# Kernel tuning notes

Measured on AMD Instinct MI355X. Metric: run time of the kernel, lower is better.

## Reference

```python
import jax, jax.numpy as jnp
import numpy as np

B, N, HN, HE, H = 8, 128, 256, 128, 8
DH = HN // H
P = N * (N - 1) // 2


def _ln(x, g, b, eps=1e-5):
    m = jnp.mean(x, axis=-1, keepdims=True)
    v = jnp.mean((x - m) ** 2, axis=-1, keepdims=True)
    return (x - m) * jax.lax.rsqrt(v + eps) * g + b


def setup_inputs() -> dict:
    key = jax.random.key(0)
    ks = jax.random.split(key, 16)
    i1, i2 = np.triu_indices(N, k=1)  # all unordered pairs, P = N(N-1)/2
    s = lambda fan: 1.0 / np.sqrt(fan)
    return {
        "node_feat": jax.random.normal(ks[0], (B, N, HN), jnp.float32),
        "edge_feat": jax.random.normal(ks[1], (B, P, HE), jnp.float32),
        "x_idx1": jnp.asarray(i1, jnp.int32),
        "x_idx2": jnp.asarray(i2, jnp.int32),
        "mask_valid": jax.random.bernoulli(ks[2], 0.9, (B, P)).astype(jnp.float32),
        "Wqkv": jax.random.normal(ks[3], (HN, 3 * HN), jnp.float32) * s(HN),
        "bqkv": jnp.zeros((3 * HN,), jnp.float32),
        "Wev": jax.random.normal(ks[4], (HE, HN), jnp.float32) * s(HE),
        "bev": jnp.zeros((HN,), jnp.float32),
        "Wea": jax.random.normal(ks[5], (HE, H), jnp.float32) * s(HE),
        "bea": jnp.zeros((H,), jnp.float32),
        "Wo": jax.random.normal(ks[6], (2 * HN, HN), jnp.float32) * s(2 * HN),
        "bo": jnp.zeros((HN,), jnp.float32),
        "Wsk": jax.random.normal(ks[7], (HN, 2 * HN), jnp.float32) * s(HN),
        "bsk": jnp.zeros((2 * HN,), jnp.float32),
        "gn": jnp.ones((HN,), jnp.float32),
        "bn": jnp.zeros((HN,), jnp.float32),
        "ge": jnp.ones((HE,), jnp.float32),
        "be": jnp.zeros((HE,), jnp.float32),
    }


def reference(node_feat, edge_feat, x_idx1, x_idx2, mask_valid,
              Wqkv, bqkv, Wev, bev, Wea, bea, Wo, bo, Wsk, bsk,
              gn, bn, ge, be):
    n_in = _ln(node_feat, gn, bn)                      # [B,N,HN]
    e_in = _ln(edge_feat, ge, be)                      # [B,P,HE]
    q, k, v = jnp.split(n_in @ Wqkv + bqkv, 3, axis=-1)
    to_h = lambda t: t.reshape(B, -1, H, DH).transpose(0, 2, 1, 3)
    q, k, v = to_h(q), to_h(k), to_h(v)                # [B,H,N,DH]
    e_val = to_h(e_in @ Wev + bev)                     # [B,H,P,DH]
    e_adj = (e_in @ Wea + bea).transpose(0, 2, 1)      # [B,H,P]

    scale = DH ** -0.5
    logits = jnp.einsum('bhqd,bhkd->bhqk', q, k) * scale  # [B,H,N,N]
    # per-pair logits; torch stacks [qk, edge_adj] then sums -> just add
    l_node1 = logits[:, :, x_idx1, x_idx2] + e_adj     # node i1 attends to i2
    l_node2 = logits[:, :, x_idx2, x_idx1] + e_adj     # node i2 attends to i1
    v_node1 = e_val + v[:, :, x_idx2]                  # value node i1 receives
    v_node2 = e_val + v[:, :, x_idx1]

    # group the 2P directed edges by destination node (= torch cat+sort+reshape)
    cat_idx = jnp.concatenate([x_idx1, x_idx2])        # [2P]
    order = jnp.argsort(cat_idx)                       # stable sort
    gl = jnp.concatenate([l_node1, l_node2], axis=2)[:, :, order].reshape(B, H, N, N - 1)
    gv = jnp.concatenate([v_node1, v_node2], axis=2)[:, :, order].reshape(B, H, N, N - 1, DH)
    gm = jnp.concatenate([mask_valid, mask_valid], axis=1)[:, order].reshape(B, N, N - 1)[:, None]  # [B,1,N,N-1]

    gl = jnp.where(gm == 0.0, -9e15, gl)
    probs = jax.nn.softmax(gl, axis=3)
    probs = probs * jnp.any(gm != 0.0, axis=3, keepdims=True).astype(probs.dtype)
    attn = jnp.einsum('bhnk,bhnkd->bhnd', probs, gv)   # [B,H,N,DH]
    attn = attn.transpose(0, 2, 1, 3).reshape(B, N, HN)

    comb = jax.nn.gelu(jnp.concatenate([n_in, attn], axis=-1) @ Wo + bo, approximate=False)
    val, gate = jnp.split(comb @ Wsk + bsk, 2, axis=-1)
    g = jax.nn.sigmoid(gate)
    return node_feat * (1.0 - g) + val * g
```

## Files before the change

### kernel.cpp

```cpp
#include <hip/hip_runtime.h>
#include <hip/hip_bf16.h>
#include <math.h>

#define BB 8
#define NN 128
#define HN 256
#define HE 128
#define NH 8
#define DH 32
#define PP 8128
#define BP (BB*PP)

typedef __hip_bfloat16 bf16;
typedef __hip_bfloat162 bf162;
typedef __attribute__((ext_vector_type(8))) short bf16x8;
typedef __attribute__((ext_vector_type(4))) float f32x4;

__device__ __forceinline__ float bf2f(bf16 x){ return __bfloat162float(x); }
__device__ __forceinline__ float bfraw2f(short u){
  return __uint_as_float(((unsigned)(unsigned short)u) << 16);
}

__device__ __forceinline__ float wave_sum(float v){
  #pragma unroll
  for (int off=32; off>=1; off>>=1) v += __shfl_xor(v, off, 64);
  return v;
}
__device__ __forceinline__ float g16_sum(float v){
  #pragma unroll
  for (int off=8; off>=1; off>>=1) v += __shfl_xor(v, off, 16);
  return v;
}

__device__ __forceinline__ int pair_idx(int a, int c){
  int i = a < c ? a : c;
  int j = a < c ? c : a;
  return ((i*(255 - i))>>1) + (j - i - 1);
}

#define C_NODE 0LL
#define C_MASK 262144LL
#define C_WQKV 327168LL
#define C_BQKV 523776LL
#define C_WEV  524544LL
#define C_BEV  557312LL
#define C_WEA  557568LL
#define C_BEA  558592LL
#define C_WO   558600LL
#define C_BO   689672LL
#define C_WSK  689928LL
#define C_BSK  821000LL
#define C_GN   821512LL
#define C_BN   821768LL
#define C_GE   822024LL
#define C_BE   822152LL
#define IOFF   822400LL
#define TOT8   102785
#define CONVBLKS 402
#define I_NIN  0LL
#define I_Q    262144LL
#define I_K    524288LL
#define I_V    786432LL
#define I_ATTN 1048576LL
#define I_COMB 1310720LL
#define I_EA2  1572864LL
#define I_XG   2093056LL
#define I_WT   14577664LL
#define I_WOB  14594048LL
#define I_WSKB 14659584LL
#define I_FLG  14725120LL

struct SrcPtrs { const void* p[16]; };

__global__ __launch_bounds__(256) void k_convert(SrcPtrs sp, float* __restrict__ dst,
                                                 int* __restrict__ flags,
                                                 const unsigned short* __restrict__ nodeRaw,
                                                 const void* __restrict__ rawWev,
                                                 bf16* __restrict__ Wt,
                                                 const void* __restrict__ rawWo,
                                                 const void* __restrict__ rawWsk,
                                                 bf16* __restrict__ WoB,
                                                 bf16* __restrict__ WskB)
{
  __shared__ int sbad;
  if (threadIdx.x == 0) sbad = 0;
  __syncthreads();
  {
    int bad = 0;
    for (int i = threadIdx.x; i < 1024; i += 256){
      unsigned e = (nodeRaw[i] >> 7) & 0xFFu;
      if (e >= 194u) bad = 1;
    }
    if (bad) sbad = 1;
  }
  __syncthreads();
  const int f32 = sbad;
  if (blockIdx.x == 0 && threadIdx.x == 0) flags[0] = f32;

  if (blockIdx.x >= CONVBLKS + 128){
    int o = (blockIdx.x - (CONVBLKS + 128))*256 + threadIdx.x;
    const void* src = (o < 16384) ? rawWo : rawWsk;
    bf16* dw = (o < 16384) ? WoB : WskB;
    int lo = (o < 16384) ? o : o - 16384;
    if (f32){
      const float4* s4 = (const float4*)src;
      float4 a0 = s4[2*lo], a1 = s4[2*lo+1];
      union { float4 f; bf16 h[8]; } cv;
      cv.h[0]=__float2bfloat16(a0.x); cv.h[1]=__float2bfloat16(a0.y);
      cv.h[2]=__float2bfloat16(a0.z); cv.h[3]=__float2bfloat16(a0.w);
      cv.h[4]=__float2bfloat16(a1.x); cv.h[5]=__float2bfloat16(a1.y);
      cv.h[6]=__float2bfloat16(a1.z); cv.h[7]=__float2bfloat16(a1.w);
      *reinterpret_cast<float4*>(dw + lo*8) = cv.f;
    } else {
      *reinterpret_cast<float4*>(dw + lo*8) = ((const float4*)src)[lo];
    }
    return;
  }

  if (blockIdx.x >= CONVBLKS){
    int idx = (blockIdx.x - CONVBLKS)*256 + threadIdx.x;
    float v = f32 ? ((const float*)rawWev)[idx]
                  : bfraw2f(((const short*)rawWev)[idx]);
    Wt[(idx & 255)*128 + (idx >> 8)] = __float2bfloat16(v);
    return;
  }

  int o = blockIdx.x*256 + threadIdx.x;
  if (o >= TOT8) return;
  const int cum[17] = {0,32768,40896,65472,65568,69664,69696,69824,69825,
                       86209,86241,102625,102689,102721,102753,102769,102785};
  int s = 0;
  #pragma unroll
  for (int i = 1; i <= 15; i++) if (o >= cum[i]) s = i;
  const int li = o - cum[s];
  float4 r0, r1;
  if (f32){
    const float4* src = (const float4*)sp.p[s];
    r0 = src[2*li]; r1 = src[2*li+1];
  } else {
    union { float4 f; unsigned short u[8]; } cv;
    cv.f = ((const float4*)sp.p[s])[li];
    r0.x = __uint_as_float((unsigned)cv.u[0] << 16);
    r0.y = __uint_as_float((unsigned)cv.u[1] << 16);
    r0.z = __uint_as_float((unsigned)cv.u[2] << 16);
    r0.w = __uint_as_float((unsigned)cv.u[3] << 16);
    r1.x = __uint_as_float((unsigned)cv.u[4] << 16);
    r1.y = __uint_as_float((unsigned)cv.u[5] << 16);
    r1.z = __uint_as_float((unsigned)cv.u[6] << 16);
    r1.w = __uint_as_float((unsigned)cv.u[7] << 16);
  }
  float4* d = (float4*)(dst + (long long)cum[s]*8);
  d[2*li]   = r0;
  d[2*li+1] = r1;
}

__global__ __launch_bounds__(256) void k1_node_ln_qkv(
    const float* __restrict__ cnode, const float* __restrict__ cWqkv,
    const float* __restrict__ cbqkv, const float* __restrict__ cgn, const float* __restrict__ cbn,
    float* __restrict__ nin_ws, float* __restrict__ q_ws, float* __restrict__ k_ws,
    float* __restrict__ v_ws)
{
  __shared__ float xln[4][HN];
  const int t = threadIdx.x, wv = t>>6, lane = t&63;
  const int cb = blockIdx.x % 3;
  const int g0 = (blockIdx.x / 3) * 4;
  {
    int g = g0 + wv;
    float x[4];
    #pragma unroll
    for (int i=0;i<4;i++) x[i] = cnode[g*HN + lane + 64*i];
    float s = x[0]+x[1]+x[2]+x[3];
    s = wave_sum(s);
    float m = s * (1.0f/HN);
    float q = 0.f;
    #pragma unroll
    for (int i=0;i<4;i++){ float d = x[i]-m; q += d*d; }
    q = wave_sum(q);
    float rstd = rsqrtf(fmaxf(q*(1.0f/HN), 0.f) + 1e-5f);
    #pragma unroll
    for (int i=0;i<4;i++){
      int c = lane + 64*i;
      float y = (x[i]-m)*rstd*cgn[c] + cbn[c];
      xln[wv][c] = y;
      if (cb == 0) nin_ws[g*HN + c] = y;
    }
  }
  __syncthreads();
  const int col = cb*256 + t;
  float acc[4];
  {
    float bb = cbqkv[col];
    #pragma unroll
    for (int r=0;r<4;r++) acc[r] = bb;
  }
  for (int k=0;k<HN;k+=4){
    float4 xv[4];
    #pragma unroll
    for (int r=0;r<4;r++) xv[r] = *reinterpret_cast<const float4*>(&xln[r][k]);
    #pragma unroll
    for (int kk=0;kk<4;kk++){
      float w = cWqkv[(k+kk)*768 + col];
      #pragma unroll
      for (int r=0;r<4;r++) acc[r] = fmaf((&xv[r].x)[kk], w, acc[r]);
    }
  }
  if (cb == 2){
    #pragma unroll
    for (int r=0;r<4;r++) v_ws[(long)(g0+r)*HN + t] = acc[r];
  } else {
    float* dstp = (cb == 0) ? q_ws : k_ws;
    const int h = t>>5, d = t&31;
    #pragma unroll
    for (int r=0;r<4;r++){
      int g = g0 + r;
      int b = g>>7, n = g&127;
      dstp[((b*NH + h)*NN + n)*DH + d] = acc[r];
    }
  }
}

__global__ __launch_bounds__(256) void k2a_edge_ln(
    const void* __restrict__ edge_raw, const float* __restrict__ cWea,
    const float* __restrict__ cbea, const float* __restrict__ cge,
    const float* __restrict__ cbe, const float* __restrict__ cmask,
    bf16* __restrict__ xg, float* __restrict__ ea2, const int* __restrict__ flags)
{
  __shared__ float xlnS[16][136];
  __shared__ float part[128];
  const int t = threadIdx.x;
  const int R0 = blockIdx.x*16;
  const int b = R0 / PP;
  const int p0 = R0 - b*PP;
  const int f32 = flags[0];
  {
    int r = t>>4, sub = t&15;
    long base = (long)(R0 + r)*HE + sub*8;
    float x[8];
    if (f32){
      const float* cef = (const float*)edge_raw + base;
      float4 a0 = *reinterpret_cast<const float4*>(cef);
      float4 a1 = *reinterpret_cast<const float4*>(cef + 4);
      x[0]=a0.x; x[1]=a0.y; x[2]=a0.z; x[3]=a0.w;
      x[4]=a1.x; x[5]=a1.y; x[6]=a1.z; x[7]=a1.w;
    } else {
      union { float4 f; short u[8]; } cv;
      cv.f = *reinterpret_cast<const float4*>((const bf16*)edge_raw + base);
      #pragma unroll
      for (int i=0;i<8;i++) x[i] = bfraw2f(cv.u[i]);
    }
    float s = 0.f;
    #pragma unroll
    for (int i=0;i<8;i++) s += x[i];
    s = g16_sum(s);
    float m = s*(1.0f/HE);
    float q = 0.f;
    #pragma unroll
    for (int i=0;i<8;i++){ float dd = x[i]-m; q += dd*dd; }
    q = g16_sum(q);
    float rstd = rsqrtf(fmaxf(q*(1.0f/HE), 0.f) + 1e-5f);
    #pragma unroll
    for (int i=0;i<8;i++){
      int c = sub*8 + i;
      xlnS[r][c] = (x[i]-m)*rstd*cge[c] + cbe[c];
    }
  }
  __syncthreads();
  {
    int r = t>>4, c0 = (t&15)*8;
    union { float4 f; bf16 h[8]; } o;
    #pragma unroll
    for (int i=0;i<8;i++) o.h[i] = __float2bfloat16(xlnS[r][c0+i]);
    *reinterpret_cast<float4*>(xg + (long)(R0 + r)*HE + c0) = o.f;
  }
  {
    const int c = t & 7, r = (t>>3) & 15, half = t>>7;
    const int pid = r*8 + c;
    float s = half ? 0.0f : cbea[c];
    const int k0 = half*64;
    #pragma unroll 8
    for (int k=k0; k<k0+64; k++) s = fmaf(xlnS[r][k], cWea[k*NH + c], s);
    if (half){ part[pid] = s; }
    __syncthreads();
    if (!half){
      s += part[pid];
      int p = p0 + r;
      float mk = cmask[b*PP + p];
      ea2[((long)b*PP + p)*8 + c] = (mk != 0.0f) ? s : -9e15f;
    }
  }
}

__global__ __launch_bounds__(256, 4) void k3_attn(
    const float* __restrict__ q_ws,
    const float* __restrict__ k_ws,
    const float* __restrict__ v_ws,
    const bf16* __restrict__ xg,
    const float* __restrict__ ea2,
    const bf16* __restrict__ Wt,
    const float* __restrict__ cbev,
    float* __restrict__ attn)
{
  __shared__ __align__(16) bf16  xgS[128][128];
  __shared__ __align__(16) float sS[8][128];
  const int t = threadIdx.x;
  const int bid = blockIdx.x;
  const int swz = (bid & 7)*128 + (bid >> 3);
  const int n = swz & 127, b = swz >> 7;
  const int h = t >> 5, ln = t & 31;

  float4 qv[8];
  const float* qb = q_ws + (((long)b*NH + h)*NN + n)*DH;
  #pragma unroll
  for (int d4=0; d4<8; d4++) qv[d4] = *reinterpret_cast<const float4*>(qb + d4*4);
  float eav[4];
  const float* eab = ea2 + (long)b*PP*8;
  #pragma unroll
  for (int j=0;j<4;j++){
    int m = ln + 32*j;
    int ms = (m == n) ? (m ^ 1) : m;
    eav[j] = eab[(long)pair_idx(n, ms)*8 + h];
  }
  const bf16* xgb = xg + (long)b*PP*HE;
  const int rowb = t >> 4, seg = t & 15;
  float4 xr[8];
  #pragma unroll
  for (int it=0; it<8; ++it){
    int row = it*16 + rowb;
    int ms = (row == n) ? (row ^ 1) : row;
    int pr = pair_idx(n, ms);
    xr[it] = *reinterpret_cast<const float4*>(xgb + (long)pr*HE + seg*8);
  }

  const float scale = 0.17677669529663687f;
  const float* kb = k_ws + ((long)b*NH + h)*NN*DH;
  float l[4];
  float mx = -INFINITY;
  int valid = 0;
  #pragma unroll
  for (int j=0;j<4;j++){
    int m = ln + 32*j;
    const float* kr = kb + m*DH;
    float dot = 0.f;
    #pragma unroll
    for (int d4=0; d4<8; d4++){
      float4 kv = *reinterpret_cast<const float4*>(kr + d4*4);
      dot = fmaf(qv[d4].x, kv.x, dot);
      dot = fmaf(qv[d4].y, kv.y, dot);
      dot = fmaf(qv[d4].z, kv.z, dot);
      dot = fmaf(qv[d4].w, kv.w, dot);
    }
    bool self = (m == n);
    l[j] = self ? -INFINITY : fmaf(dot, scale, eav[j]);
    if (!self && eav[j] > -8.9e15f) valid = 1;
    mx = fmaxf(mx, l[j]);
  }
  #pragma unroll
  for (int off=16; off>=1; off>>=1) mx = fmaxf(mx, __shfl_xor(mx, off, 32));
  float e[4], s = 0.f;
  #pragma unroll
  for (int j=0;j<4;j++){ e[j] = __expf(l[j]-mx); s += e[j]; }
  float av = valid ? 1.f : 0.f;
  #pragma unroll
  for (int off=16; off>=1; off>>=1){
    s  += __shfl_xor(s,  off, 32);
    av += __shfl_xor(av, off, 32);
  }
  float inv = (av > 0.f) ? (1.0f/s) : 0.f;
  float pj0 = e[0]*inv, pj1 = e[1]*inv, pj2 = e[2]*inv, pj3 = e[3]*inv;

  #pragma unroll
  for (int it=0; it<8; ++it){
    int row = it*16 + rowb;
    *reinterpret_cast<float4*>(&xgS[row][seg*8]) = xr[it];
  }
  __syncthreads();

  const float* vb = v_ws + (long)b*NN*HN + h*DH + ln;
  float S0=0.f,S1=0.f,S2=0.f,S3=0.f,T=0.f;
  #pragma unroll
  for (int j=0;j<4;j++){
    float pcur = (j==0) ? pj0 : (j==1) ? pj1 : (j==2) ? pj2 : pj3;
    #pragma unroll 2
    for (int mm=0; mm<32; mm+=4){
      #pragma unroll
      for (int i=0;i<4;i++){
        int m = j*32 + mm + i;
        float pm = __shfl(pcur, mm + i, 32);
        short4 xv = *reinterpret_cast<const short4*>(&xgS[m][ln*4]);
        S0 = fmaf(pm, bfraw2f(xv.x), S0);
        S1 = fmaf(pm, bfraw2f(xv.y), S1);
        S2 = fmaf(pm, bfraw2f(xv.z), S2);
        S3 = fmaf(pm, bfraw2f(xv.w), S3);
        T  = fmaf(pm, vb[m*HN], T);
      }
    }
  }
  {
    float4 sv; sv.x=S0; sv.y=S1; sv.z=S2; sv.w=S3;
    *reinterpret_cast<float4*>(&sS[h][ln*4]) = sv;
  }
  __syncthreads();

  float acc = T + ((av > 0.f) ? cbev[h*DH + ln] : 0.f);
  const bf16* wr = Wt + (h*DH + ln)*HE;
  #pragma unroll 4
  for (int k0=0;k0<128;k0+=8){
    float4 sa = *reinterpret_cast<const float4*>(&sS[h][k0]);
    float4 sb = *reinterpret_cast<const float4*>(&sS[h][k0+4]);
    bf16x8 wv = *reinterpret_cast<const bf16x8*>(wr + k0);
    acc = fmaf(sa.x, bfraw2f(wv[0]), acc);
    acc = fmaf(sa.y, bfraw2f(wv[1]), acc);
    acc = fmaf(sa.z, bfraw2f(wv[2]), acc);
    acc = fmaf(sa.w, bfraw2f(wv[3]), acc);
    acc = fmaf(sb.x, bfraw2f(wv[4]), acc);
    acc = fmaf(sb.y, bfraw2f(wv[5]), acc);
    acc = fmaf(sb.z, bfraw2f(wv[6]), acc);
    acc = fmaf(sb.w, bfraw2f(wv[7]), acc);
  }
  attn[((long)b*NN + n)*HN + h*DH + ln] = acc;
}

__global__ __launch_bounds__(256) void k4_wo_gelu(
    const float* __restrict__ nin_ws, const float* __restrict__ attn,
    const bf16* __restrict__ WoB, const float* __restrict__ cbo,
    float* __restrict__ comb)
{
  __shared__ float xc[4][512];
  __shared__ float ps[3][4][64];
  const int t = threadIdx.x;
  const int g0 = (blockIdx.x >> 2) * 4;
  const int cq = blockIdx.x & 3;
  {
    int r = t>>6, c0 = (t&63)*8;
    const float* src = (c0 < 256) ? (nin_ws + (long)(g0+r)*HN + c0)
                                  : (attn + (long)(g0+r)*HN + (c0-256));
    float4 a0 = *reinterpret_cast<const float4*>(src);
    float4 a1 = *reinterpret_cast<const float4*>(src+4);
    *reinterpret_cast<float4*>(&xc[r][c0]) = a0;
    *reinterpret_cast<float4*>(&xc[r][c0+4]) = a1;
  }
  __syncthreads();
  const int cidx = t & 63, ks = t >> 6;
  const int col = cq*64 + cidx;
  float acc[4] = {0.f,0.f,0.f,0.f};
  const int k0 = ks*128;
  #pragma unroll 4
  for (int k=k0; k<k0+128; k++){
    float w = bf2f(WoB[k*HN + col]);
    #pragma unroll
    for (int r=0;r<4;r++) acc[r] = fmaf(xc[r][k], w, acc[r]);
  }
  if (ks){
    #pragma unroll
    for (int r=0;r<4;r++) ps[ks-1][r][cidx] = acc[r];
  }
  __syncthreads();
  if (!ks){
    float bb = cbo[col];
    #pragma unroll
    for (int r=0;r<4;r++){
      float x = acc[r] + bb + ps[0][r][cidx] + ps[1][r][cidx] + ps[2][r][cidx];
      comb[(long)(g0+r)*HN + col] = 0.5f*x*(1.0f + erff(x*0.7071067811865475f));
    }
  }
}

__global__ __launch_bounds__(256) void k5_sk_gate(
    const float* __restrict__ comb, const float* __restrict__ cnode,
    const bf16* __restrict__ WskB, const float* __restrict__ cbsk,
    void* __restrict__ out, const int* __restrict__ flags)
{
  __shared__ float xc[4][HN];
  __shared__ float psv[3][4][64];
  __shared__ float psg[3][4][64];
  const int t = threadIdx.x;
  const int g0 = (blockIdx.x >> 2) * 4;
  const int cq = blockIdx.x & 3;
  {
    int r = t>>6, c0 = (t&63)*4;
    *reinterpret_cast<float4*>(&xc[r][c0]) =
        *reinterpret_cast<const float4*>(comb + (long)(g0+r)*HN + c0);
  }
  __syncthreads();
  const int cidx = t & 63, ks = t >> 6;
  const int col = cq*64 + cidx;
  float av[4] = {0.f,0.f,0.f,0.f}, ag[4] = {0.f,0.f,0.f,0.f};
  const int k0 = ks*64;
  #pragma unroll 4
  for (int k=k0; k<k0+64; k++){
    float wv = bf2f(WskB[k*512 + col]);
    float wg = bf2f(WskB[k*512 + col + 256]);
    #pragma unroll
    for (int r=0;r<4;r++){
      float xr = xc[r][k];
      av[r] = fmaf(xr, wv, av[r]);
      ag[r] = fmaf(xr, wg, ag[r]);
    }
  }
  if (ks){
    #pragma unroll
    for (int r=0;r<4;r++){ psv[ks-1][r][cidx] = av[r]; psg[ks-1][r][cidx] = ag[r]; }
  }
  __syncthreads();
  if (!ks){
    const int f32 = flags[0];
    float bv = cbsk[col], bg = cbsk[col+256];
    #pragma unroll
    for (int r=0;r<4;r++){
      float v = av[r] + bv + psv[0][r][cidx] + psv[1][r][cidx] + psv[2][r][cidx];
      float g = ag[r] + bg + psg[0][r][cidx] + psg[1][r][cidx] + psg[2][r][cidx];
      float gg = 1.0f/(1.0f + __expf(-g));
      float nf = cnode[(long)(g0+r)*HN + col];
      float res = nf*(1.0f - gg) + v*gg;
      if (f32) ((float*)out)[(long)(g0+r)*HN + col] = res;
      else ((bf16*)out)[(long)(g0+r)*HN + col] = __float2bfloat16(res);
    }
  }
}

extern "C" void kernel_launch(void* const* d_in, const int* in_sizes, int n_inputs,
                              void* d_out, int out_size, void* d_ws, size_t ws_size,
                              hipStream_t stream)
{
  float* ws = (float*)d_ws;
  float* c_node = ws + C_NODE;
  float* c_mask = ws + C_MASK;
  float* c_Wqkv = ws + C_WQKV;
  float* c_bqkv = ws + C_BQKV;
  float* c_bev  = ws + C_BEV;
  float* c_Wea  = ws + C_WEA;
  float* c_bea  = ws + C_BEA;
  float* c_bo   = ws + C_BO;
  float* c_bsk  = ws + C_BSK;
  float* c_gn   = ws + C_GN;
  float* c_bn   = ws + C_BN;
  float* c_ge   = ws + C_GE;
  float* c_be   = ws + C_BE;
  float* base   = ws + IOFF;
  float* nin_ws  = base + I_NIN;
  float* q_ws    = base + I_Q;
  float* k_ws    = base + I_K;
  float* v_ws    = base + I_V;
  float* attn_ws = base + I_ATTN;
  float* comb_ws = base + I_COMB;
  float* ea2_ws  = base + I_EA2;
  bf16*  xg_ws   = (bf16*)(base + I_XG);
  bf16*  wt_ws   = (bf16*)(base + I_WT);
  bf16*  wob_ws  = (bf16*)(base + I_WOB);
  bf16*  wskb_ws = (bf16*)(base + I_WSKB);
  int*   flags   = (int*)(base + I_FLG);

  SrcPtrs sp;
  sp.p[0]  = d_in[0];
  sp.p[1]  = d_in[4];
  sp.p[2]  = d_in[5];
  sp.p[3]  = d_in[6];
  sp.p[4]  = d_in[7];
  sp.p[5]  = d_in[8];
  sp.p[6]  = d_in[9];
  sp.p[7]  = d_in[10];
  sp.p[8]  = d_in[11];
  sp.p[9]  = d_in[12];
  sp.p[10] = d_in[13];
  sp.p[11] = d_in[14];
  sp.p[12] = d_in[15];
  sp.p[13] = d_in[16];
  sp.p[14] = d_in[17];
  sp.p[15] = d_in[18];

  k_convert<<<CONVBLKS + 256, 256, 0, stream>>>(sp, ws, flags,
                                                (const unsigned short*)d_in[0],
                                                d_in[7], wt_ws,
                                                d_in[11], d_in[13],
                                                wob_ws, wskb_ws);
  k1_node_ln_qkv<<<768, 256, 0, stream>>>(c_node, c_Wqkv, c_bqkv, c_gn, c_bn,
                                          nin_ws, q_ws, k_ws, v_ws);
  k2a_edge_ln<<<BP/16, 256, 0, stream>>>(d_in[1], c_Wea, c_bea, c_ge, c_be, c_mask,
                                         xg_ws, ea2_ws, flags);
  k3_attn<<<BB*NN, 256, 0, stream>>>(q_ws, k_ws, v_ws, xg_ws, ea2_ws, wt_ws, c_bev,
                                     attn_ws);
  k4_wo_gelu<<<1024, 256, 0, stream>>>(nin_ws, attn_ws, wob_ws, c_bo, comb_ws);
  k5_sk_gate<<<1024, 256, 0, stream>>>(comb_ws, c_node, wskb_ws, c_bsk, d_out, flags);
}
```

Baseline: 198.0 us.

## Merge conversion, node LN/QKV and edge LN into one launch; fuse Wo and gate kernels

Removes the separate fp32 staging kernel: the node, edge and weight-prep stages now read raw inputs directly, with dtype conversion done inline, and run as block ranges of a single launch. Each block detects the input dtype itself. The Wo+GELU and skip/gate kernels are merged so the comb intermediate stays in shared memory. The cost is fewer blocks (256) with the full K loop per thread and no split-K in the merged kernel, which may reduce parallelism in that stage.

```diff
diff --git a/kernel.cpp b/kernel.cpp
--- a/kernel.cpp
+++ b/kernel.cpp
@@ -38,25 +38,10 @@
   return ((i*(255 - i))>>1) + (j - i - 1);
 }
 
-#define C_NODE 0LL
-#define C_MASK 262144LL
-#define C_WQKV 327168LL
-#define C_BQKV 523776LL
-#define C_WEV  524544LL
 #define C_BEV  557312LL
-#define C_WEA  557568LL
-#define C_BEA  558592LL
-#define C_WO   558600LL
 #define C_BO   689672LL
-#define C_WSK  689928LL
 #define C_BSK  821000LL
-#define C_GN   821512LL
-#define C_BN   821768LL
-#define C_GE   822024LL
-#define C_BE   822152LL
 #define IOFF   822400LL
-#define TOT8   102785
-#define CONVBLKS 402
 #define I_NIN  0LL
 #define I_Q    262144LL
 #define I_K    524288LL
@@ -70,36 +55,221 @@
 #define I_WSKB 14659584LL
 #define I_FLG  14725120LL
 
+#define EDGEBLKS 4064
+#define NODEBLKS 768
+#define PREPBLKS 257
+
 struct SrcPtrs { const void* p[16]; };
 
-__global__ __launch_bounds__(256) void k_convert(SrcPtrs sp, float* __restrict__ dst,
-                                                 int* __restrict__ flags,
-                                                 const unsigned short* __restrict__ nodeRaw,
-                                                 const void* __restrict__ rawWev,
-                                                 bf16* __restrict__ Wt,
-                                                 const void* __restrict__ rawWo,
-                                                 const void* __restrict__ rawWsk,
-                                                 bf16* __restrict__ WoB,
-                                                 bf16* __restrict__ WskB)
+__device__ __forceinline__ int detect_f32(const unsigned short* nodeRaw, int* sbad){
+  if (threadIdx.x == 0) *sbad = 0;
+  __syncthreads();
+  int bad = 0;
+  for (int i = threadIdx.x; i < 1024; i += 256){
+    unsigned e = (nodeRaw[i] >> 7) & 0xFFu;
+    if (e >= 194u) bad = 1;
+  }
+  if (bad) *sbad = 1;
+  __syncthreads();
+  return *sbad;
+}
+
+__device__ __forceinline__ float dualf(const void* p, long i, int f32){
+  return f32 ? ((const float*)p)[i] : bfraw2f(((const short*)p)[i]);
+}
+
+__global__ __launch_bounds__(256) void kA(
+    SrcPtrs sp, const void* __restrict__ edge_raw,
+    float* __restrict__ nin_ws, float* __restrict__ q_ws, float* __restrict__ k_ws,
+    float* __restrict__ v_ws, bf16* __restrict__ xg, float* __restrict__ ea2,
+    bf16* __restrict__ Wt, bf16* __restrict__ WoB, bf16* __restrict__ WskB,
+    float* __restrict__ ws, int* __restrict__ flags)
 {
-  __shared__ int sbad;
-  if (threadIdx.x == 0) sbad = 0;
-  __syncthreads();
-  {
-    int bad = 0;
-    for (int i = threadIdx.x; i < 1024; i += 256){
-      unsigned e = (nodeRaw[i] >> 7) & 0xFFu;
-      if (e >= 194u) bad = 1;
-    }
-    if (bad) sbad = 1;
-  }
-  __syncthreads();
-  const int f32 = sbad;
-  if (blockIdx.x == 0 && threadIdx.x == 0) flags[0] = f32;
-
-  if (blockIdx.x >= CONVBLKS + 128){
-    int o = (blockIdx.x - (CONVBLKS + 128))*256 + threadIdx.x;
-    const void* src = (o < 16384) ? rawWo : rawWsk;
+  __shared__ __align__(16) float smemF[3330];
+  int* sbad = (int*)&smemF[3328];
+  const int t = threadIdx.x;
+  int bb = blockIdx.x;
+
+  if (bb < EDGEBLKS){
+    const int f32 = detect_f32((const unsigned short*)sp.p[0], sbad);
+    float* xlnS = smemF;
+    float* part = smemF + 2176;
+    float* WeaS = smemF + 2304;
+    {
+      int i0 = t*4;
+      if (f32){
+        *reinterpret_cast<float4*>(&WeaS[i0]) =
+            *reinterpret_cast<const float4*>((const float*)sp.p[6] + i0);
+      } else {
+        union { float2 f; short u[4]; } cv;
+        cv.f = *reinterpret_cast<const float2*>((const short*)sp.p[6] + i0);
+        WeaS[i0]   = bfraw2f(cv.u[0]); WeaS[i0+1] = bfraw2f(cv.u[1]);
+        WeaS[i0+2] = bfraw2f(cv.u[2]); WeaS[i0+3] = bfraw2f(cv.u[3]);
+      }
+    }
+    const int R0 = bb*16;
+    const int b = R0 / PP;
+    const int p0 = R0 - b*PP;
+    {
+      int r = t>>4, sub = t&15;
+      long base = (long)(R0 + r)*HE + sub*8;
+      float x[8];
+      if (f32){
+        const float* cef = (const float*)edge_raw + base;
+        float4 a0 = *reinterpret_cast<const float4*>(cef);
+        float4 a1 = *reinterpret_cast<const float4*>(cef + 4);
+        x[0]=a0.x; x[1]=a0.y; x[2]=a0.z; x[3]=a0.w;
+        x[4]=a1.x; x[5]=a1.y; x[6]=a1.z; x[7]=a1.w;
+      } else {
+        union { float4 f; short u[8]; } cv;
+        cv.f = *reinterpret_cast<const float4*>((const bf16*)edge_raw + base);
+        #pragma unroll
+        for (int i=0;i<8;i++) x[i] = bfraw2f(cv.u[i]);
+      }
+      float s = 0.f;
+      #pragma unroll
+      for (int i=0;i<8;i++) s += x[i];
+      s = g16_sum(s);
+      float m = s*(1.0f/HE);
+      float q = 0.f;
+      #pragma unroll
+      for (int i=0;i<8;i++){ float dd = x[i]-m; q += dd*dd; }
+      q = g16_sum(q);
+      float rstd = rsqrtf(fmaxf(q*(1.0f/HE), 0.f) + 1e-5f);
+      #pragma unroll
+      for (int i=0;i<8;i++){
+        int c = sub*8 + i;
+        float gev = dualf(sp.p[14], c, f32);
+        float bev = dualf(sp.p[15], c, f32);
+        xlnS[r*136 + c] = (x[i]-m)*rstd*gev + bev;
+      }
+    }
+    __syncthreads();
+    {
+      int r = t>>4, c0 = (t&15)*8;
+      union { float4 f; bf16 h[8]; } o;
+      #pragma unroll
+      for (int i=0;i<8;i++) o.h[i] = __float2bfloat16(xlnS[r*136 + c0+i]);
+      *reinterpret_cast<float4*>(xg + (long)(R0 + r)*HE + c0) = o.f;
+    }
+    {
+      const int c = t & 7, r = (t>>3) & 15, half = t>>7;
+      const int pid = r*8 + c;
+      float s = half ? 0.0f : dualf(sp.p[7], c, f32);
+      const int k0 = half*64;
+      #pragma unroll 8
+      for (int k=k0; k<k0+64; k++) s = fmaf(xlnS[r*136 + k], WeaS[k*NH + c], s);
+      if (half){ part[pid] = s; }
+      __syncthreads();
+      if (!half){
+        s += part[pid];
+        int p = p0 + r;
+        float mk = dualf(sp.p[1], (long)b*PP + p, f32);
+        ea2[((long)b*PP + p)*8 + c] = (mk != 0.0f) ? s : -9e15f;
+      }
+    }
+    return;
+  }
+  bb -= EDGEBLKS;
+
+  if (bb < NODEBLKS){
+    const int f32 = detect_f32((const unsigned short*)sp.p[0], sbad);
+    float* xln = smemF;
+    const int wv = t>>6, lane = t&63;
+    const int cb = bb % 3;
+    const int g0 = (bb / 3) * 4;
+    {
+      int g = g0 + wv;
+      float x[4];
+      if (f32){
+        const float* cn = (const float*)sp.p[0];
+        #pragma unroll
+        for (int i=0;i<4;i++) x[i] = cn[(long)g*HN + lane + 64*i];
+      } else {
+        const short* cn = (const short*)sp.p[0];
+        #pragma unroll
+        for (int i=0;i<4;i++) x[i] = bfraw2f(cn[(long)g*HN + lane + 64*i]);
+      }
+      float s = x[0]+x[1]+x[2]+x[3];
+      s = wave_sum(s);
+      float m = s * (1.0f/HN);
+      float q = 0.f;
+      #pragma unroll
+      for (int i=0;i<4;i++){ float d = x[i]-m; q += d*d; }
+      q = wave_sum(q);
+      float rstd = rsqrtf(fmaxf(q*(1.0f/HN), 0.f) + 1e-5f);
+      #pragma unroll
+      for (int i=0;i<4;i++){
+        int c = lane + 64*i;
+        float gnv = dualf(sp.p[12], c, f32);
+        float bnv = dualf(sp.p[13], c, f32);
+        float y = (x[i]-m)*rstd*gnv + bnv;
+        xln[wv*HN + c] = y;
+        if (cb == 0) nin_ws[(long)g*HN + c] = y;
+      }
+    }
+    __syncthreads();
+    const int col = cb*256 + t;
+    float acc[4];
+    {
+      float bb0 = dualf(sp.p[3], col, f32);
+      #pragma unroll
+      for (int r=0;r<4;r++) acc[r] = bb0;
+    }
+    if (f32){
+      const float* W = (const float*)sp.p[2];
+      for (int k=0;k<HN;k+=4){
+        float4 xv[4];
+        #pragma unroll
+        for (int r=0;r<4;r++) xv[r] = *reinterpret_cast<const float4*>(&xln[r*HN + k]);
+        #pragma unroll
+        for (int kk=0;kk<4;kk++){
+          float w = W[(long)(k+kk)*768 + col];
+          #pragma unroll
+          for (int r=0;r<4;r++) acc[r] = fmaf((&xv[r].x)[kk], w, acc[r]);
+        }
+      }
+    } else {
+      const short* W = (const short*)sp.p[2];
+      for (int k=0;k<HN;k+=4){
+        float4 xv[4];
+        #pragma unroll
+        for (int r=0;r<4;r++) xv[r] = *reinterpret_cast<const float4*>(&xln[r*HN + k]);
+        #pragma unroll
+        for (int kk=0;kk<4;kk++){
+          float w = bfraw2f(W[(long)(k+kk)*768 + col]);
+          #pragma unroll
+          for (int r=0;r<4;r++) acc[r] = fmaf((&xv[r].x)[kk], w, acc[r]);
+        }
+      }
+    }
+    if (cb == 2){
+      #pragma unroll
+      for (int r=0;r<4;r++) v_ws[(long)(g0+r)*HN + t] = acc[r];
+    } else {
+      float* dstp = (cb == 0) ? q_ws : k_ws;
+      const int h = t>>5, d = t&31;
+      #pragma unroll
+      for (int r=0;r<4;r++){
+        int g = g0 + r;
+        int b = g>>7, n = g&127;
+        dstp[((b*NH + h)*NN + n)*DH + d] = acc[r];
+      }
+    }
+    return;
+  }
+  bb -= NODEBLKS;
+
+  const int f32 = detect_f32((const unsigned short*)sp.p[0], sbad);
+  if (bb < 128){
+    int idx = bb*256 + t;
+    float v = dualf(sp.p[4], idx, f32);
+    Wt[(idx & 255)*128 + (idx >> 8)] = __float2bfloat16(v);
+    return;
+  }
+  if (bb < 256){
+    int o = (bb-128)*256 + t;
+    const void* src = (o < 16384) ? sp.p[8] : sp.p[10];
     bf16* dw = (o < 16384) ? WoB : WskB;
     int lo = (o < 16384) ? o : o - 16384;
     if (f32){
@@ -116,177 +286,13 @@
     }
     return;
   }
-
-  if (blockIdx.x >= CONVBLKS){
-    int idx = (blockIdx.x - CONVBLKS)*256 + threadIdx.x;
-    float v = f32 ? ((const float*)rawWev)[idx]
-                  : bfraw2f(((const short*)rawWev)[idx]);
-    Wt[(idx & 255)*128 + (idx >> 8)] = __float2bfloat16(v);
-    return;
-  }
-
-  int o = blockIdx.x*256 + threadIdx.x;
-  if (o >= TOT8) return;
-  const int cum[17] = {0,32768,40896,65472,65568,69664,69696,69824,69825,
-                       86209,86241,102625,102689,102721,102753,102769,102785};
-  int s = 0;
-  #pragma unroll
-  for (int i = 1; i <= 15; i++) if (o >= cum[i]) s = i;
-  const int li = o - cum[s];
-  float4 r0, r1;
-  if (f32){
-    const float4* src = (const float4*)sp.p[s];
-    r0 = src[2*li]; r1 = src[2*li+1];
-  } else {
-    union { float4 f; unsigned short u[8]; } cv;
-    cv.f = ((const float4*)sp.p[s])[li];
-    r0.x = __uint_as_float((unsigned)cv.u[0] << 16);
-    r0.y = __uint_as_float((unsigned)cv.u[1] << 16);
-    r0.z = __uint_as_float((unsigned)cv.u[2] << 16);
-    r0.w = __uint_as_float((unsigned)cv.u[3] << 16);
-    r1.x = __uint_as_float((unsigned)cv.u[4] << 16);
-    r1.y = __uint_as_float((unsigned)cv.u[5] << 16);
-    r1.z = __uint_as_float((unsigned)cv.u[6] << 16);
-    r1.w = __uint_as_float((unsigned)cv.u[7] << 16);
-  }
-  float4* d = (float4*)(dst + (long long)cum[s]*8);
-  d[2*li]   = r0;
-  d[2*li+1] = r1;
-}
-
-__global__ __launch_bounds__(256) void k1_node_ln_qkv(
-    const float* __restrict__ cnode, const float* __restrict__ cWqkv,
-    const float* __restrict__ cbqkv, const float* __restrict__ cgn, const float* __restrict__ cbn,
-    float* __restrict__ nin_ws, float* __restrict__ q_ws, float* __restrict__ k_ws,
-    float* __restrict__ v_ws)
-{
-  __shared__ float xln[4][HN];
-  const int t = threadIdx.x, wv = t>>6, lane = t&63;
-  const int cb = blockIdx.x % 3;
-  const int g0 = (blockIdx.x / 3) * 4;
-  {
-    int g = g0 + wv;
-    float x[4];
-    #pragma unroll
-    for (int i=0;i<4;i++) x[i] = cnode[g*HN + lane + 64*i];
-    float s = x[0]+x[1]+x[2]+x[3];
-    s = wave_sum(s);
-    float m = s * (1.0f/HN);
-    float q = 0.f;
-    #pragma unroll
-    for (int i=0;i<4;i++){ float d = x[i]-m; q += d*d; }
-    q = wave_sum(q);
-    float rstd = rsqrtf(fmaxf(q*(1.0f/HN), 0.f) + 1e-5f);
-    #pragma unroll
-    for (int i=0;i<4;i++){
-      int c = lane + 64*i;
-      float y = (x[i]-m)*rstd*cgn[c] + cbn[c];
-      xln[wv][c] = y;
-      if (cb == 0) nin_ws[g*HN + c] = y;
-    }
-  }
-  __syncthreads();
-  const int col = cb*256 + t;
-  float acc[4];
-  {
-    float bb = cbqkv[col];
-    #pragma unroll
-    for (int r=0;r<4;r++) acc[r] = bb;
-  }
-  for (int k=0;k<HN;k+=4){
-    float4 xv[4];
-    #pragma unroll
-    for (int r=0;r<4;r++) xv[r] = *reinterpret_cast<const float4*>(&xln[r][k]);
-    #pragma unroll
-    for (int kk=0;kk<4;kk++){
-      float w = cWqkv[(k+kk)*768 + col];
-      #pragma unroll
-      for (int r=0;r<4;r++) acc[r] = fmaf((&xv[r].x)[kk], w, acc[r]);
-    }
-  }
-  if (cb == 2){
-    #pragma unroll
-    for (int r=0;r<4;r++) v_ws[(long)(g0+r)*HN + t] = acc[r];
-  } else {
-    float* dstp = (cb == 0) ? q_ws : k_ws;
-    const int h = t>>5, d = t&31;
-    #pragma unroll
-    for (int r=0;r<4;r++){
-      int g = g0 + r;
-      int b = g>>7, n = g&127;
-      dstp[((b*NH + h)*NN + n)*DH + d] = acc[r];
-    }
-  }
-}
-
-__global__ __launch_bounds__(256) void k2a_edge_ln(
-    const void* __restrict__ edge_raw, const float* __restrict__ cWea,
-    const float* __restrict__ cbea, const float* __restrict__ cge,
-    const float* __restrict__ cbe, const float* __restrict__ cmask,
-    bf16* __restrict__ xg, float* __restrict__ ea2, const int* __restrict__ flags)
-{
-  __shared__ float xlnS[16][136];
-  __shared__ float part[128];
-  const int t = threadIdx.x;
-  const int R0 = blockIdx.x*16;
-  const int b = R0 / PP;
-  const int p0 = R0 - b*PP;
-  const int f32 = flags[0];
-  {
-    int r = t>>4, sub = t&15;
-    long base = (long)(R0 + r)*HE + sub*8;
-    float x[8];
-    if (f32){
-      const float* cef = (const float*)edge_raw + base;
-      float4 a0 = *reinterpret_cast<const float4*>(cef);
-      float4 a1 = *reinterpret_cast<const float4*>(cef + 4);
-      x[0]=a0.x; x[1]=a0.y; x[2]=a0.z; x[3]=a0.w;
-      x[4]=a1.x; x[5]=a1.y; x[6]=a1.z; x[7]=a1.w;
-    } else {
-      union { float4 f; short u[8]; } cv;
-      cv.f = *reinterpret_cast<const float4*>((const bf16*)edge_raw + base);
-      #pragma unroll
-      for (int i=0;i<8;i++) x[i] = bfraw2f(cv.u[i]);
-    }
-    float s = 0.f;
-    #pragma unroll
-    for (int i=0;i<8;i++) s += x[i];
-    s = g16_sum(s);
-    float m = s*(1.0f/HE);
-    float q = 0.f;
-    #pragma unroll
-    for (int i=0;i<8;i++){ float dd = x[i]-m; q += dd*dd; }
-    q = g16_sum(q);
-    float rstd = rsqrtf(fmaxf(q*(1.0f/HE), 0.f) + 1e-5f);
-    #pragma unroll
-    for (int i=0;i<8;i++){
-      int c = sub*8 + i;
-      xlnS[r][c] = (x[i]-m)*rstd*cge[c] + cbe[c];
-    }
-  }
-  __syncthreads();
-  {
-    int r = t>>4, c0 = (t&15)*8;
-    union { float4 f; bf16 h[8]; } o;
-    #pragma unroll
-    for (int i=0;i<8;i++) o.h[i] = __float2bfloat16(xlnS[r][c0+i]);
-    *reinterpret_cast<float4*>(xg + (long)(R0 + r)*HE + c0) = o.f;
-  }
-  {
-    const int c = t & 7, r = (t>>3) & 15, half = t>>7;
-    const int pid = r*8 + c;
-    float s = half ? 0.0f : cbea[c];
-    const int k0 = half*64;
-    #pragma unroll 8
-    for (int k=k0; k<k0+64; k++) s = fmaf(xlnS[r][k], cWea[k*NH + c], s);
-    if (half){ part[pid] = s; }
-    __syncthreads();
-    if (!half){
-      s += part[pid];
-      int p = p0 + r;
-      float mk = cmask[b*PP + p];
-      ea2[((long)b*PP + p)*8 + c] = (mk != 0.0f) ? s : -9e15f;
-    }
+  if (t == 0) flags[0] = f32;
+  for (int i = t; i < 1024; i += 256){
+    const void* src; float* dst; int li;
+    if (i < 256){ src = sp.p[5];  dst = ws + C_BEV; li = i; }
+    else if (i < 512){ src = sp.p[9];  dst = ws + C_BO;  li = i-256; }
+    else { src = sp.p[11]; dst = ws + C_BSK; li = i-512; }
+    dst[li] = dualf(src, li, f32);
   }
 }
 
@@ -420,16 +426,17 @@
   attn[((long)b*NN + n)*HN + h*DH + ln] = acc;
 }
 
-__global__ __launch_bounds__(256) void k4_wo_gelu(
+__global__ __launch_bounds__(256) void k45(
     const float* __restrict__ nin_ws, const float* __restrict__ attn,
     const bf16* __restrict__ WoB, const float* __restrict__ cbo,
-    float* __restrict__ comb)
+    const bf16* __restrict__ WskB, const float* __restrict__ cbsk,
+    const void* __restrict__ cnode_raw, void* __restrict__ out,
+    const int* __restrict__ flags)
 {
-  __shared__ float xc[4][512];
-  __shared__ float ps[3][4][64];
+  __shared__ __align__(16) float xc[4][512];
+  __shared__ __align__(16) float cbS[4][256];
   const int t = threadIdx.x;
-  const int g0 = (blockIdx.x >> 2) * 4;
-  const int cq = blockIdx.x & 3;
+  const int g0 = blockIdx.x * 4;
   {
     int r = t>>6, c0 = (t&63)*8;
     const float* src = (c0 < 256) ? (nin_ws + (long)(g0+r)*HN + c0)
@@ -440,81 +447,52 @@
     *reinterpret_cast<float4*>(&xc[r][c0+4]) = a1;
   }
   __syncthreads();
-  const int cidx = t & 63, ks = t >> 6;
-  const int col = cq*64 + cidx;
-  float acc[4] = {0.f,0.f,0.f,0.f};
-  const int k0 = ks*128;
+  const int col = t;
+  float acc[4];
+  {
+    float bb0 = cbo[col];
+    #pragma unroll
+    for (int r=0;r<4;r++) acc[r] = bb0;
+  }
   #pragma unroll 4
-  for (int k=k0; k<k0+128; k++){
+  for (int k=0;k<512;k++){
     float w = bf2f(WoB[k*HN + col]);
     #pragma unroll
     for (int r=0;r<4;r++) acc[r] = fmaf(xc[r][k], w, acc[r]);
   }
-  if (ks){
+  #pragma unroll
+  for (int r=0;r<4;r++){
+    float x = acc[r];
+    cbS[r][col] = 0.5f*x*(1.0f + erff(x*0.7071067811865475f));
+  }
+  __syncthreads();
+  float av[4], ag[4];
+  {
+    float bv = cbsk[col], bg = cbsk[col+256];
     #pragma unroll
-    for (int r=0;r<4;r++) ps[ks-1][r][cidx] = acc[r];
-  }
-  __syncthreads();
-  if (!ks){
-    float bb = cbo[col];
-    #pragma unroll
-    for (int r=0;r<4;r++){
-      float x = acc[r] + bb + ps[0][r][cidx] + ps[1][r][cidx] + ps[2][r][cidx];
-      comb[(long)(g0+r)*HN + col] = 0.5f*x*(1.0f + erff(x*0.7071067811865475f));
-    }
-  }
-}
-
-__global__ __launch_bounds__(256) void k5_sk_gate(
-    const float* __restrict__ comb, const float* __restrict__ cnode,
-    const bf16* __restrict__ WskB, const float* __restrict__ cbsk,
-    void* __restrict__ out, const int* __restrict__ flags)
-{
-  __shared__ float xc[4][HN];
-  __shared__ float psv[3][4][64];
-  __shared__ float psg[3][4][64];
-  const int t = threadIdx.x;
-  const int g0 = (blockIdx.x >> 2) * 4;
-  const int cq = blockIdx.x & 3;
-  {
-    int r = t>>6, c0 = (t&63)*4;
-    *reinterpret_cast<float4*>(&xc[r][c0]) =
-        *reinterpret_cast<const float4*>(comb + (long)(g0+r)*HN + c0);
-  }
-  __syncthreads();
-  const int cidx = t & 63, ks = t >> 6;
-  const int col = cq*64 + cidx;
-  float av[4] = {0.f,0.f,0.f,0.f}, ag[4] = {0.f,0.f,0.f,0.f};
-  const int k0 = ks*64;
+    for (int r=0;r<4;r++){ av[r] = bv; ag[r] = bg; }
+  }
   #pragma unroll 4
-  for (int k=k0; k<k0+64; k++){
+  for (int k=0;k<256;k++){
     float wv = bf2f(WskB[k*512 + col]);
     float wg = bf2f(WskB[k*512 + col + 256]);
     #pragma unroll
     for (int r=0;r<4;r++){
-      float xr = xc[r][k];
+      float xr = cbS[r][k];
       av[r] = fmaf(xr, wv, av[r]);
       ag[r] = fmaf(xr, wg, ag[r]);
     }
   }
-  if (ks){
-    #pragma unroll
-    for (int r=0;r<4;r++){ psv[ks-1][r][cidx] = av[r]; psg[ks-1][r][cidx] = ag[r]; }
-  }
-  __syncthreads();
-  if (!ks){
-    const int f32 = flags[0];
-    float bv = cbsk[col], bg = cbsk[col+256];
-    #pragma unroll
-    for (int r=0;r<4;r++){
-      float v = av[r] + bv + psv[0][r][cidx] + psv[1][r][cidx] + psv[2][r][cidx];
-      float g = ag[r] + bg + psg[0][r][cidx] + psg[1][r][cidx] + psg[2][r][cidx];
-      float gg = 1.0f/(1.0f + __expf(-g));
-      float nf = cnode[(long)(g0+r)*HN + col];
-      float res = nf*(1.0f - gg) + v*gg;
-      if (f32) ((float*)out)[(long)(g0+r)*HN + col] = res;
-      else ((bf16*)out)[(long)(g0+r)*HN + col] = __float2bfloat16(res);
-    }
+  const int f32 = flags[0];
+  #pragma unroll
+  for (int r=0;r<4;r++){
+    float gg = 1.0f/(1.0f + __expf(-ag[r]));
+    long idx = (long)(g0+r)*HN + col;
+    float nf = f32 ? ((const float*)cnode_raw)[idx]
+                   : bfraw2f(((const short*)cnode_raw)[idx]);
+    float res = nf*(1.0f - gg) + av[r]*gg;
+    if (f32) ((float*)out)[idx] = res;
+    else ((bf16*)out)[idx] = __float2bfloat16(res);
   }
 }
 
@@ -523,26 +501,12 @@
                               hipStream_t stream)
 {
   float* ws = (float*)d_ws;
-  float* c_node = ws + C_NODE;
-  float* c_mask = ws + C_MASK;
-  float* c_Wqkv = ws + C_WQKV;
-  float* c_bqkv = ws + C_BQKV;
-  float* c_bev  = ws + C_BEV;
-  float* c_Wea  = ws + C_WEA;
-  float* c_bea  = ws + C_BEA;
-  float* c_bo   = ws + C_BO;
-  float* c_bsk  = ws + C_BSK;
-  float* c_gn   = ws + C_GN;
-  float* c_bn   = ws + C_BN;
-  float* c_ge   = ws + C_GE;
-  float* c_be   = ws + C_BE;
   float* base   = ws + IOFF;
   float* nin_ws  = base + I_NIN;
   float* q_ws    = base + I_Q;
   float* k_ws    = base + I_K;
   float* v_ws    = base + I_V;
   float* attn_ws = base + I_ATTN;
-  float* comb_ws = base + I_COMB;
   float* ea2_ws  = base + I_EA2;
   bf16*  xg_ws   = (bf16*)(base + I_XG);
   bf16*  wt_ws   = (bf16*)(base + I_WT);
@@ -568,17 +532,11 @@
   sp.p[14] = d_in[17];
   sp.p[15] = d_in[18];
 
-  k_convert<<<CONVBLKS + 256, 256, 0, stream>>>(sp, ws, flags,
-                                                (const unsigned short*)d_in[0],
-                                                d_in[7], wt_ws,
-                                                d_in[11], d_in[13],
-                                                wob_ws, wskb_ws);
-  k1_node_ln_qkv<<<768, 256, 0, stream>>>(c_node, c_Wqkv, c_bqkv, c_gn, c_bn,
-                                          nin_ws, q_ws, k_ws, v_ws);
-  k2a_edge_ln<<<BP/16, 256, 0, stream>>>(d_in[1], c_Wea, c_bea, c_ge, c_be, c_mask,
-                                         xg_ws, ea2_ws, flags);
-  k3_attn<<<BB*NN, 256, 0, stream>>>(q_ws, k_ws, v_ws, xg_ws, ea2_ws, wt_ws, c_bev,
-                                     attn_ws);
-  k4_wo_gelu<<<1024, 256, 0, stream>>>(nin_ws, attn_ws, wob_ws, c_bo, comb_ws);
-  k5_sk_gate<<<1024, 256, 0, stream>>>(comb_ws, c_node, wskb_ws, c_bsk, d_out, flags);
-}
+  kA<<<EDGEBLKS + NODEBLKS + PREPBLKS, 256, 0, stream>>>(
+      sp, d_in[1], nin_ws, q_ws, k_ws, v_ws, xg_ws, ea2_ws,
+      wt_ws, wob_ws, wskb_ws, ws, flags);
+  k3_attn<<<BB*NN, 256, 0, stream>>>(q_ws, k_ws, v_ws, xg_ws, ea2_ws, wt_ws,
+                                     ws + C_BEV, attn_ws);
+  k45<<<256, 256, 0, stream>>>(nin_ws, attn_ws, wob_ws, ws + C_BO,
+                               wskb_ws, ws + C_BSK, d_in[0], d_out, flags);
+}
```

After: 251.2 us. 26.8% more time.
